# Optimization experiments

Measured on AMD Instinct MI355X. Metric: run time of the kernel, lower is better.

The kernel has to match this reference:

```python
import jax, jax.numpy as jnp
import numpy as np

# Model hyperparams (must match init_kwargs)
N_CATEGORIES = 1000
EMBED_DIM = 128
N_DEMAND = 8
HIDDEN = 128
B, L, N_ITEMS = 16, 50, 8192


def setup_inputs() -> dict:
    key = jax.random.key(0)
    ks = jax.random.split(key, 12)
    inp = {}
    inp["input"] = jax.random.randint(ks[0], (B, L), 0, N_CATEGORIES)
    inp["candidate_pool_category"] = jax.random.randint(ks[1], (N_ITEMS,), 0, N_CATEGORIES)
    inp["session_last_catgy_index"] = jax.random.randint(ks[2], (B,), 0, L)
    inp["mask_catgy"] = jnp.ones((B, L), dtype=jnp.float32)
    # Learned parameters (torch Linear stored as (in, out) so y = x @ W + b)
    emb = 0.02 * jax.random.normal(ks[3], (N_CATEGORIES, EMBED_DIM), dtype=jnp.float32)
    inp["emb_table"] = emb.at[0].set(0.0)  # padding_idx=0
    sd = 1.0 / np.sqrt(EMBED_DIM)
    sh = 1.0 / np.sqrt(HIDDEN)
    inp["Wd"] = sd * jax.random.normal(ks[4], (EMBED_DIM, N_DEMAND * HIDDEN), dtype=jnp.float32)
    inp["Wk"] = sd * jax.random.normal(ks[5], (EMBED_DIM, HIDDEN), dtype=jnp.float32)
    inp["bk"] = sd * jax.random.normal(ks[6], (HIDDEN,), dtype=jnp.float32)
    inp["W1"] = (1.0 / np.sqrt(2 * HIDDEN)) * jax.random.normal(ks[7], (2 * HIDDEN, HIDDEN), dtype=jnp.float32)
    inp["b1"] = sh * jax.random.normal(ks[8], (HIDDEN,), dtype=jnp.float32)
    inp["w_score"] = sh * jax.random.normal(ks[9], (HIDDEN,), dtype=jnp.float32)
    inp["Wc"] = sh * jax.random.normal(ks[10], (HIDDEN, N_CATEGORIES), dtype=jnp.float32)
    inp["bc"] = sh * jax.random.normal(ks[11], (N_CATEGORIES,), dtype=jnp.float32)
    return inp


def reference(input, candidate_pool_category, session_last_catgy_index, mask_catgy,
              emb_table, Wd, Wk, bk, W1, b1, w_score, Wc, bc):
    B_, L_ = input.shape
    h = Wk.shape[1]
    D = Wd.shape[1] // h

    emb = emb_table[input]                      # (B, L, d)  (dropout = identity at eval)
    emb_cand = emb_table[candidate_pool_category]  # (N, d)

    hidden_key = emb @ Wk + bk                  # (B, L, h)
    hidden_demand = (emb @ Wd).reshape(B_, L_, D, h)
    # demand_agg == 'exp': log(sum(exp(.), axis=seq))
    agg = jax.nn.logsumexp(hidden_demand, axis=1)   # (B, D, h)

    # demand similarity loss: mean off-diagonal cosine similarity between demands
    hn = agg / (jnp.linalg.norm(agg, axis=-1, keepdims=True) + 1e-12)
    sim = jnp.einsum('bdh,beh->bde', hn, hn)
    off = sim * (1.0 - jnp.eye(D, dtype=sim.dtype))
    demand_sim_loss = jnp.sum(off) / (B_ * D * (D - 1))

    hidden_key_cand = emb_cand @ Wk + bk        # (N, h)

    # MLP score: cat([demand, key]) @ W1 == demand @ W1[:h] + key @ W1[h:]
    Wd1, Wk1 = W1[:h], W1[h:]
    pd = agg @ Wd1                              # (B, D, h)
    pk = hidden_key @ Wk1                       # (B, L, h)
    s = jax.nn.relu(pd[:, None, :, :] + pk[:, :, None, :] + b1)  # (B, L, D, h)
    # torch does .view(B, D, L) on a contiguous (B, L, D) tensor -> raw reshape (kept faithful)
    demand_score = (s @ w_score).reshape(B_, D, L_)              # (B, D, L)

    pkc = hidden_key_cand @ Wk1                 # (N, h)
    sc = jax.nn.relu(pd[:, :, None, :] + pkc[None, None, :, :] + b1)  # (B, D, N, h)
    demand_score_candidate = sc @ w_score       # (B, D, N)

    # predict_catgy ('mlp'): linear head over aggregated demand (reconstructed; body truncated in source)
    catgy_score = agg @ Wc + bc                 # (B, D, n_categories)

    return (catgy_score, demand_score, demand_score_candidate, emb, emb_cand, demand_sim_loss)
```

## Files before the change

kernel.cpp:

```cpp
#include <hip/hip_runtime.h>
#include <hip/hip_bf16.h>

#define NB 16
#define NL 50
#define ND 8
#define NH 128
#define NC 1000
#define NI 8192

#define OFF_CAT  0
#define OFF_DS   128000
#define OFF_DSC  134400
#define OFF_EMB  1182976
#define OFF_EMBC 1285376
#define OFF_LOSS 2333952

#define WS_SPART 0
#define WS_PK    81920
#define WS_PKCT  184320
#define WS_WP    1232896
#define WS_BP    1249280
#define WS_AGG   1249408
#define WS_PD2   1265792

__global__ __launch_bounds__(256) void k_stage0(
    const int* __restrict__ inp, const float* __restrict__ emb_table,
    const float* __restrict__ Wd, const float* __restrict__ Wk,
    const float* __restrict__ bk, const float* __restrict__ W1,
    float* __restrict__ ws_wp, float* __restrict__ ws_bp,
    float* __restrict__ ws_spart, float* __restrict__ out_loss)
{
    const int bx = blockIdx.x;
    const int t = threadIdx.x;
    const int c = t & 127, g = t >> 7;
    __shared__ __align__(16) float smem[1536];

    if (bx < 64) {
        float* wk_s = smem;
        const float* __restrict__ Wk1 = W1 + 128 * 128;
        const int r0 = bx * 2;
        wk_s[t] = Wk[(r0 + g) * 128 + c];
        __syncthreads();
        float a = 0.f;
        for (int k = 0; k < 128; k += 4) {
            #pragma unroll
            for (int j = 0; j < 4; ++j)
                a = fmaf(wk_s[g * 128 + k + j], Wk1[(k + j) * 128 + c], a);
        }
        ws_wp[(r0 + g) * 128 + c] = a;
    } else if (bx == 64) {
        float* wk_s = smem;
        const float* __restrict__ Wk1 = W1 + 128 * 128;
        if (t < 128) wk_s[t] = bk[t];
        __syncthreads();
        if (t < 128) {
            float a = 0.f;
            for (int k = 0; k < 128; k += 4) {
                #pragma unroll
                for (int j = 0; j < 4; ++j)
                    a = fmaf(wk_s[k + j], Wk1[(k + j) * 128 + t], a);
            }
            ws_bp[t] = a;
        }
        if (t == 0) out_loss[0] = 0.f;
    } else {
        const int idx = bx - 65;
        const int bd = idx / 5, chunk = idx % 5;
        const int b = bd >> 3, d = bd & 7;
        float* se = smem;
        float* ss = smem + 1280;
        for (int ii = t; ii < 1280; ii += 256) {
            const int row = ii >> 7, col = ii & 127;
            const int cat = inp[b * NL + chunk * 10 + row];
            se[ii] = emb_table[cat * 128 + col];
        }
        __syncthreads();
        const float* __restrict__ wp = Wd + d * 128 + c;
        float acc[5] = {0.f, 0.f, 0.f, 0.f, 0.f};
        const int l0 = g * 5;
        for (int k = 0; k < 128; k += 4) {
            const float w0 = wp[(k + 0) * 1024], w1 = wp[(k + 1) * 1024];
            const float w2 = wp[(k + 2) * 1024], w3 = wp[(k + 3) * 1024];
            #pragma unroll
            for (int li = 0; li < 5; ++li) {
                const float4 e4 = *reinterpret_cast<const float4*>(&se[(l0 + li) * 128 + k]);
                acc[li] = fmaf(e4.w, w3, fmaf(e4.z, w2, fmaf(e4.y, w1, fmaf(e4.x, w0, acc[li]))));
            }
        }
        float s = 0.f;
        #pragma unroll
        for (int li = 0; li < 5; ++li) s += expf(acc[li]);
        ss[g * 128 + c] = s;
        __syncthreads();
        if (g == 0)
            ws_spart[(bd * 5 + chunk) * 128 + c] = ss[c] + ss[128 + c];
    }
}

__global__ __launch_bounds__(256) void k_stage1(
    const int* __restrict__ inp, const int* __restrict__ cand,
    const float* __restrict__ emb_table, const float* __restrict__ W1,
    const float* __restrict__ b1, const float* __restrict__ Wc,
    const float* __restrict__ bc, const float* __restrict__ ws_wp,
    const float* __restrict__ ws_bp, const float* __restrict__ ws_spart,
    float* __restrict__ out_emb, float* __restrict__ out_embc,
    float* __restrict__ out_cat, float* __restrict__ ws_pk,
    float* __restrict__ ws_pkcT, float* __restrict__ ws_agg,
    float* __restrict__ ws_pd2)
{
    const int bx = blockIdx.x;
    const int t = threadIdx.x;
    const int c = t & 127, g = t >> 7;
    __shared__ __align__(16) float smem[2176];

    if (bx < 100) {
        const int r0 = bx * 8;
        float* e_s = smem;
        #pragma unroll
        for (int r = 0; r < 4; ++r) {
            const int gr = g * 4 + r;
            const int cat = inp[r0 + gr];
            const float v = emb_table[cat * 128 + c];
            e_s[gr * 128 + c] = v;
            out_emb[(r0 + gr) * 128 + c] = v;
        }
        __syncthreads();
        const float bpv = ws_bp[c];
        float acc[4] = {bpv, bpv, bpv, bpv};
        for (int k = 0; k < 128; k += 4) {
            const float w0 = ws_wp[(k + 0) * 128 + c], w1 = ws_wp[(k + 1) * 128 + c];
            const float w2 = ws_wp[(k + 2) * 128 + c], w3 = ws_wp[(k + 3) * 128 + c];
            #pragma unroll
            for (int r = 0; r < 4; ++r) {
                const float4 e4 = *reinterpret_cast<const float4*>(&e_s[(g * 4 + r) * 128 + k]);
                acc[r] = fmaf(e4.w, w3, fmaf(e4.z, w2, fmaf(e4.y, w1, fmaf(e4.x, w0, acc[r]))));
            }
        }
        #pragma unroll
        for (int r = 0; r < 4; ++r) ws_pk[(r0 + g * 4 + r) * 128 + c] = acc[r];
    } else if (bx < 612) {
        const int i0 = (bx - 100) * 16;
        float* e_s = smem;
        #pragma unroll
        for (int r = 0; r < 8; ++r) {
            const int gr = g * 8 + r;
            const int cat = cand[i0 + gr];
            const float v = emb_table[cat * 128 + c];
            e_s[gr * 128 + c] = v;
            out_embc[(i0 + gr) * 128 + c] = v;
        }
        __syncthreads();
        const float bpv = ws_bp[c];
        float acc[8];
        #pragma unroll
        for (int r = 0; r < 8; ++r) acc[r] = bpv;
        for (int k = 0; k < 128; k += 4) {
            const float w0 = ws_wp[(k + 0) * 128 + c], w1 = ws_wp[(k + 1) * 128 + c];
            const float w2 = ws_wp[(k + 2) * 128 + c], w3 = ws_wp[(k + 3) * 128 + c];
            #pragma unroll
            for (int r = 0; r < 8; ++r) {
                const float4 e4 = *reinterpret_cast<const float4*>(&e_s[(g * 8 + r) * 128 + k]);
                acc[r] = fmaf(e4.w, w3, fmaf(e4.z, w2, fmaf(e4.y, w1, fmaf(e4.x, w0, acc[r]))));
            }
        }
        __syncthreads();
        float* tb = smem;
        #pragma unroll
        for (int r = 0; r < 8; ++r) tb[(g * 8 + r) * 132 + c] = acc[r];
        __syncthreads();
        #pragma unroll
        for (int p = 0; p < 2; ++p) {
            const int h = p * 64 + (t >> 2);
            const int ib = (t & 3) * 4;
            const float4 v = make_float4(tb[(ib + 0) * 132 + h], tb[(ib + 1) * 132 + h],
                                         tb[(ib + 2) * 132 + h], tb[(ib + 3) * 132 + h]);
            *reinterpret_cast<float4*>(&ws_pkcT[(size_t)h * NI + i0 + ib]) = v;
        }
    } else {
        const int bd = bx - 612;
        float* a_s = smem;
        if (g == 0) {
            float s = 0.f;
            #pragma unroll
            for (int ch = 0; ch < 5; ++ch) s += ws_spart[(bd * 5 + ch) * 128 + c];
            const float av = logf(s);
            a_s[c] = av;
            ws_agg[bd * 128 + c] = av;
        }
        __syncthreads();
        if (g == 0) {
            float acc = b1[c];
            for (int k = 0; k < 128; k += 4) {
                acc = fmaf(a_s[k + 0], W1[(k + 0) * 128 + c], acc);
                acc = fmaf(a_s[k + 1], W1[(k + 1) * 128 + c], acc);
                acc = fmaf(a_s[k + 2], W1[(k + 2) * 128 + c], acc);
                acc = fmaf(a_s[k + 3], W1[(k + 3) * 128 + c], acc);
            }
            ws_pd2[bd * 128 + c] = acc;
        }
        float acc4[4];
        int   col4[4];
        #pragma unroll
        for (int j = 0; j < 4; ++j) {
            const int col = t + j * 256;
            col4[j] = (col < NC) ? col : (NC - 1);
            acc4[j] = bc[col4[j]];
        }
        for (int k = 0; k < 128; ++k) {
            const float av = a_s[k];
            const float* wr = Wc + (size_t)k * NC;
            #pragma unroll
            for (int j = 0; j < 4; ++j) acc4[j] = fmaf(av, wr[col4[j]], acc4[j]);
        }
        #pragma unroll
        for (int j = 0; j < 4; ++j) {
            const int col = t + j * 256;
            if (col < NC) out_cat[bd * NC + col] = acc4[j];
        }
    }
}

__global__ __launch_bounds__(256) void k_tail3(
    const float* __restrict__ ws_agg, const float* __restrict__ ws_pd2,
    const float* __restrict__ ws_pk, const float* __restrict__ ws_pkcT,
    const float* __restrict__ w_score, float* __restrict__ out_ds,
    float* __restrict__ out_dsc, float* __restrict__ out_loss)
{
    const int bx = blockIdx.x;
    const int t = threadIdx.x;
    __shared__ __align__(16) float smem[928];
    float* pd_s = smem;
    float* ws_s = smem + 512;
    float* sp   = smem + 640;
    float* aux  = smem + 896;

    if (bx < 1024) {
        const int ichunk = bx & 31, rh = (bx >> 5) & 1, b = bx >> 6;
        const int r0 = b * 8 + rh * 4;
        const int i = ichunk * 256 + t;
        for (int j = t; j < 512; j += 256) pd_s[j] = ws_pd2[r0 * 128 + j];
        if (t < 128) ws_s[t] = w_score[t];
        __syncthreads();
        float a0 = 0.f, a1 = 0.f, a2 = 0.f, a3 = 0.f;
        const float* __restrict__ pc0 = ws_pkcT + i;
        float4 pv = make_float4(pc0[0], pc0[NI], pc0[2 * NI], pc0[3 * NI]);
        for (int h = 0; h < 128; h += 4) {
            const float4 cur = pv;
            if (h + 4 < 128) {
                const float* __restrict__ pn = ws_pkcT + (size_t)(h + 4) * NI + i;
                pv = make_float4(pn[0], pn[NI], pn[2 * NI], pn[3 * NI]);
            }
            const float4 w4 = *reinterpret_cast<const float4*>(&ws_s[h]);
            const float4 p0 = *reinterpret_cast<const float4*>(&pd_s[h]);
            const float4 p1 = *reinterpret_cast<const float4*>(&pd_s[128 + h]);
            const float4 p2 = *reinterpret_cast<const float4*>(&pd_s[256 + h]);
            const float4 p3 = *reinterpret_cast<const float4*>(&pd_s[384 + h]);
            a0 = fmaf(fmaxf(p0.x + cur.x, 0.f), w4.x, a0);
            a0 = fmaf(fmaxf(p0.y + cur.y, 0.f), w4.y, a0);
            a0 = fmaf(fmaxf(p0.z + cur.z, 0.f), w4.z, a0);
            a0 = fmaf(fmaxf(p0.w + cur.w, 0.f), w4.w, a0);
            a1 = fmaf(fmaxf(p1.x + cur.x, 0.f), w4.x, a1);
            a1 = fmaf(fmaxf(p1.y + cur.y, 0.f), w4.y, a1);
            a1 = fmaf(fmaxf(p1.z + cur.z, 0.f), w4.z, a1);
            a1 = fmaf(fmaxf(p1.w + cur.w, 0.f), w4.w, a1);
            a2 = fmaf(fmaxf(p2.x + cur.x, 0.f), w4.x, a2);
            a2 = fmaf(fmaxf(p2.y + cur.y, 0.f), w4.y, a2);
            a2 = fmaf(fmaxf(p2.z + cur.z, 0.f), w4.z, a2);
            a2 = fmaf(fmaxf(p2.w + cur.w, 0.f), w4.w, a2);
            a3 = fmaf(fmaxf(p3.x + cur.x, 0.f), w4.x, a3);
            a3 = fmaf(fmaxf(p3.y + cur.y, 0.f), w4.y, a3);
            a3 = fmaf(fmaxf(p3.z + cur.z, 0.f), w4.z, a3);
            a3 = fmaf(fmaxf(p3.w + cur.w, 0.f), w4.w, a3);
        }
        out_dsc[(size_t)(r0 + 0) * NI + i] = a0;
        out_dsc[(size_t)(r0 + 1) * NI + i] = a1;
        out_dsc[(size_t)(r0 + 2) * NI + i] = a2;
        out_dsc[(size_t)(r0 + 3) * NI + i] = a3;
    } else if (bx < 1824) {
        const int bl = bx - 1024;
        const int b = bl / 50, l = bl % 50;
        const int c = t & 127, g = t >> 7;
        const int w = t >> 6, lane = t & 63;
        float* red = aux;
        const float pkv = ws_pk[(size_t)bl * 128 + c];
        const float wv = w_score[c];
        #pragma unroll
        for (int r = 0; r < 4; ++r) {
            const int d = g * 4 + r;
            float v = fmaxf(ws_pd2[(b * 8 + d) * 128 + c] + pkv, 0.f) * wv;
            v += __shfl_down(v, 32); v += __shfl_down(v, 16); v += __shfl_down(v, 8);
            v += __shfl_down(v, 4);  v += __shfl_down(v, 2);  v += __shfl_down(v, 1);
            if (lane == 0) red[w * 4 + r] = v;
        }
        __syncthreads();
        if (t < 8) {
            const int gg = t >> 2, rr = t & 3;
            out_ds[b * 400 + l * 8 + t] = red[(2 * gg) * 4 + rr] + red[(2 * gg + 1) * 4 + rr];
        }
    } else {
        const int b = bx - 1824;
        const int c = t & 127, g = t >> 7;
        const int w = t >> 6, lane = t & 63;
        float* normp = aux;
        float* wred  = aux + 16;
        float a[4];
        #pragma unroll
        for (int r = 0; r < 4; ++r) a[r] = ws_agg[(b * 8 + g * 4 + r) * 128 + c];
        #pragma unroll
        for (int r = 0; r < 4; ++r) {
            float s = a[r] * a[r];
            s += __shfl_down(s, 32); s += __shfl_down(s, 16); s += __shfl_down(s, 8);
            s += __shfl_down(s, 4);  s += __shfl_down(s, 2);  s += __shfl_down(s, 1);
            if (lane == 0) normp[w * 4 + r] = s;
        }
        __syncthreads();
        float Sp = 0.f;
        #pragma unroll
        for (int r = 0; r < 4; ++r) {
            const float nsq = normp[(2 * g) * 4 + r] + normp[(2 * g + 1) * 4 + r];
            const float iv = 1.f / (sqrtf(nsq) + 1e-12f);
            Sp = fmaf(a[r], iv, Sp);
        }
        sp[g * 128 + c] = Sp;
        __syncthreads();
        float p = 0.f;
        if (t < 128) {
            const float S = sp[c] + sp[128 + c];
            p = S * S;
        }
        p += __shfl_down(p, 32); p += __shfl_down(p, 16); p += __shfl_down(p, 8);
        p += __shfl_down(p, 4);  p += __shfl_down(p, 2);  p += __shfl_down(p, 1);
        if (lane == 0) wred[w] = p;
        __syncthreads();
        if (t == 0) {
            float corr = 0.f;
            #pragma unroll
            for (int d = 0; d < 8; ++d) {
                const float nsq = normp[(2 * (d >> 2)) * 4 + (d & 3)] +
                                  normp[(2 * (d >> 2) + 1) * 4 + (d & 3)];
                const float iv = 1.f / (sqrtf(nsq) + 1e-12f);
                corr = fmaf(nsq, iv * iv, corr);
            }
            atomicAdd(out_loss,
                      (wred[0] + wred[1] + wred[2] + wred[3] - corr) * (1.0f / 896.0f));
        }
    }
}

extern "C" void kernel_launch(void* const* d_in, const int* in_sizes, int n_in,
                              void* d_out, int out_size, void* d_ws, size_t ws_size,
                              hipStream_t stream)
{
    const int*   input     = (const int*)d_in[0];
    const int*   cand      = (const int*)d_in[1];
    const float* emb_table = (const float*)d_in[4];
    const float* Wd        = (const float*)d_in[5];
    const float* Wk        = (const float*)d_in[6];
    const float* bk        = (const float*)d_in[7];
    const float* W1        = (const float*)d_in[8];
    const float* b1        = (const float*)d_in[9];
    const float* w_score   = (const float*)d_in[10];
    const float* Wc        = (const float*)d_in[11];
    const float* bc        = (const float*)d_in[12];

    float* out = (float*)d_out;
    float* out_cat  = out + OFF_CAT;
    float* out_ds   = out + OFF_DS;
    float* out_dsc  = out + OFF_DSC;
    float* out_emb  = out + OFF_EMB;
    float* out_embc = out + OFF_EMBC;
    float* out_loss = out + OFF_LOSS;

    float* ws       = (float*)d_ws;
    float* ws_spart = ws + WS_SPART;
    float* ws_pk    = ws + WS_PK;
    float* ws_pkcT  = ws + WS_PKCT;
    float* ws_wp    = ws + WS_WP;
    float* ws_bp    = ws + WS_BP;
    float* ws_agg   = ws + WS_AGG;
    float* ws_pd2   = ws + WS_PD2;

    k_stage0<<<705, 256, 0, stream>>>(input, emb_table, Wd, Wk, bk, W1,
                                      ws_wp, ws_bp, ws_spart, out_loss);
    k_stage1<<<740, 256, 0, stream>>>(input, cand, emb_table, W1, b1, Wc, bc,
                                      ws_wp, ws_bp, ws_spart,
                                      out_emb, out_embc, out_cat,
                                      ws_pk, ws_pkcT, ws_agg, ws_pd2);
    k_tail3<<<1840, 256, 0, stream>>>(ws_agg, ws_pd2, ws_pk, ws_pkcT, w_score,
                                      out_ds, out_dsc, out_loss);
}
```

Before: 119.7 us.

## Fuse three kernels into one persistent kernel with software grid barriers

Merges the three stage kernels into a single launch of 1024 blocks. Two atomic-counter grid barriers, reset by a memset before the launch, separate the former stages, and the tail stage loops its 1840 work items over the fixed grid. This removes the launch gaps between kernels. In exchange it adds barrier spin cost, and it deadlocks unless all 1024 blocks are resident at once (launch bounds request 4 blocks per CU).

```diff
diff --git a/kernel.cpp b/kernel.cpp
--- a/kernel.cpp
+++ b/kernel.cpp
@@ -22,18 +22,41 @@
 #define WS_BP    1249280
 #define WS_AGG   1249408
 #define WS_PD2   1265792
-
-__global__ __launch_bounds__(256) void k_stage0(
-    const int* __restrict__ inp, const float* __restrict__ emb_table,
-    const float* __restrict__ Wd, const float* __restrict__ Wk,
-    const float* __restrict__ bk, const float* __restrict__ W1,
-    float* __restrict__ ws_wp, float* __restrict__ ws_bp,
-    float* __restrict__ ws_spart, float* __restrict__ out_loss)
+#define WS_BAR   1282176
+
+#define GRID_N 1024
+
+__device__ __forceinline__ void grid_barrier(int* cnt) {
+    __syncthreads();
+    if (threadIdx.x == 0) {
+        __threadfence();
+        atomicAdd(cnt, 1);
+        while (atomicAdd(cnt, 0) < GRID_N)
+            __builtin_amdgcn_s_sleep(2);
+        __threadfence();
+    }
+    __syncthreads();
+}
+
+__global__ __launch_bounds__(256, 4) void k_all(
+    const int* __restrict__ inp, const int* __restrict__ cand,
+    const float* __restrict__ emb_table, const float* __restrict__ Wd,
+    const float* __restrict__ Wk, const float* __restrict__ bk,
+    const float* __restrict__ W1, const float* __restrict__ b1,
+    const float* __restrict__ w_score, const float* __restrict__ Wc,
+    const float* __restrict__ bc,
+    float* __restrict__ out_emb, float* __restrict__ out_embc,
+    float* __restrict__ out_cat, float* __restrict__ out_ds,
+    float* __restrict__ out_dsc, float* __restrict__ out_loss,
+    float* __restrict__ ws_pk, float* __restrict__ ws_pkcT,
+    float* __restrict__ ws_spart, float* __restrict__ ws_wp,
+    float* __restrict__ ws_bp, float* __restrict__ ws_agg,
+    float* __restrict__ ws_pd2, int* __restrict__ bar)
 {
     const int bx = blockIdx.x;
     const int t = threadIdx.x;
     const int c = t & 127, g = t >> 7;
-    __shared__ __align__(16) float smem[1536];
+    __shared__ __align__(16) float smem[2176];
 
     if (bx < 64) {
         float* wk_s = smem;
@@ -63,7 +86,7 @@
             ws_bp[t] = a;
         }
         if (t == 0) out_loss[0] = 0.f;
-    } else {
+    } else if (bx < 705) {
         const int idx = bx - 65;
         const int bd = idx / 5, chunk = idx % 5;
         const int b = bd >> 3, d = bd & 7;
@@ -95,23 +118,8 @@
         if (g == 0)
             ws_spart[(bd * 5 + chunk) * 128 + c] = ss[c] + ss[128 + c];
     }
-}
-
-__global__ __launch_bounds__(256) void k_stage1(
-    const int* __restrict__ inp, const int* __restrict__ cand,
-    const float* __restrict__ emb_table, const float* __restrict__ W1,
-    const float* __restrict__ b1, const float* __restrict__ Wc,
-    const float* __restrict__ bc, const float* __restrict__ ws_wp,
-    const float* __restrict__ ws_bp, const float* __restrict__ ws_spart,
-    float* __restrict__ out_emb, float* __restrict__ out_embc,
-    float* __restrict__ out_cat, float* __restrict__ ws_pk,
-    float* __restrict__ ws_pkcT, float* __restrict__ ws_agg,
-    float* __restrict__ ws_pd2)
-{
-    const int bx = blockIdx.x;
-    const int t = threadIdx.x;
-    const int c = t & 127, g = t >> 7;
-    __shared__ __align__(16) float smem[2176];
+
+    grid_barrier(&bar[0]);
 
     if (bx < 100) {
         const int r0 = bx * 8;
@@ -176,7 +184,7 @@
                                          tb[(ib + 2) * 132 + h], tb[(ib + 3) * 132 + h]);
             *reinterpret_cast<float4*>(&ws_pkcT[(size_t)h * NI + i0 + ib]) = v;
         }
-    } else {
+    } else if (bx < 740) {
         const int bd = bx - 612;
         float* a_s = smem;
         if (g == 0) {
@@ -218,131 +226,124 @@
             if (col < NC) out_cat[bd * NC + col] = acc4[j];
         }
     }
-}
-
-__global__ __launch_bounds__(256) void k_tail3(
-    const float* __restrict__ ws_agg, const float* __restrict__ ws_pd2,
-    const float* __restrict__ ws_pk, const float* __restrict__ ws_pkcT,
-    const float* __restrict__ w_score, float* __restrict__ out_ds,
-    float* __restrict__ out_dsc, float* __restrict__ out_loss)
-{
-    const int bx = blockIdx.x;
-    const int t = threadIdx.x;
-    __shared__ __align__(16) float smem[928];
+
+    grid_barrier(&bar[16]);
+
     float* pd_s = smem;
     float* ws_s = smem + 512;
     float* sp   = smem + 640;
     float* aux  = smem + 896;
 
-    if (bx < 1024) {
-        const int ichunk = bx & 31, rh = (bx >> 5) & 1, b = bx >> 6;
-        const int r0 = b * 8 + rh * 4;
-        const int i = ichunk * 256 + t;
-        for (int j = t; j < 512; j += 256) pd_s[j] = ws_pd2[r0 * 128 + j];
-        if (t < 128) ws_s[t] = w_score[t];
-        __syncthreads();
-        float a0 = 0.f, a1 = 0.f, a2 = 0.f, a3 = 0.f;
-        const float* __restrict__ pc0 = ws_pkcT + i;
-        float4 pv = make_float4(pc0[0], pc0[NI], pc0[2 * NI], pc0[3 * NI]);
-        for (int h = 0; h < 128; h += 4) {
-            const float4 cur = pv;
-            if (h + 4 < 128) {
-                const float* __restrict__ pn = ws_pkcT + (size_t)(h + 4) * NI + i;
-                pv = make_float4(pn[0], pn[NI], pn[2 * NI], pn[3 * NI]);
-            }
-            const float4 w4 = *reinterpret_cast<const float4*>(&ws_s[h]);
-            const float4 p0 = *reinterpret_cast<const float4*>(&pd_s[h]);
-            const float4 p1 = *reinterpret_cast<const float4*>(&pd_s[128 + h]);
-            const float4 p2 = *reinterpret_cast<const float4*>(&pd_s[256 + h]);
-            const float4 p3 = *reinterpret_cast<const float4*>(&pd_s[384 + h]);
-            a0 = fmaf(fmaxf(p0.x + cur.x, 0.f), w4.x, a0);
-            a0 = fmaf(fmaxf(p0.y + cur.y, 0.f), w4.y, a0);
-            a0 = fmaf(fmaxf(p0.z + cur.z, 0.f), w4.z, a0);
-            a0 = fmaf(fmaxf(p0.w + cur.w, 0.f), w4.w, a0);
-            a1 = fmaf(fmaxf(p1.x + cur.x, 0.f), w4.x, a1);
-            a1 = fmaf(fmaxf(p1.y + cur.y, 0.f), w4.y, a1);
-            a1 = fmaf(fmaxf(p1.z + cur.z, 0.f), w4.z, a1);
-            a1 = fmaf(fmaxf(p1.w + cur.w, 0.f), w4.w, a1);
-            a2 = fmaf(fmaxf(p2.x + cur.x, 0.f), w4.x, a2);
-            a2 = fmaf(fmaxf(p2.y + cur.y, 0.f), w4.y, a2);
-            a2 = fmaf(fmaxf(p2.z + cur.z, 0.f), w4.z, a2);
-            a2 = fmaf(fmaxf(p2.w + cur.w, 0.f), w4.w, a2);
-            a3 = fmaf(fmaxf(p3.x + cur.x, 0.f), w4.x, a3);
-            a3 = fmaf(fmaxf(p3.y + cur.y, 0.f), w4.y, a3);
-            a3 = fmaf(fmaxf(p3.z + cur.z, 0.f), w4.z, a3);
-            a3 = fmaf(fmaxf(p3.w + cur.w, 0.f), w4.w, a3);
-        }
-        out_dsc[(size_t)(r0 + 0) * NI + i] = a0;
-        out_dsc[(size_t)(r0 + 1) * NI + i] = a1;
-        out_dsc[(size_t)(r0 + 2) * NI + i] = a2;
-        out_dsc[(size_t)(r0 + 3) * NI + i] = a3;
-    } else if (bx < 1824) {
-        const int bl = bx - 1024;
-        const int b = bl / 50, l = bl % 50;
-        const int c = t & 127, g = t >> 7;
-        const int w = t >> 6, lane = t & 63;
-        float* red = aux;
-        const float pkv = ws_pk[(size_t)bl * 128 + c];
-        const float wv = w_score[c];
-        #pragma unroll
-        for (int r = 0; r < 4; ++r) {
-            const int d = g * 4 + r;
-            float v = fmaxf(ws_pd2[(b * 8 + d) * 128 + c] + pkv, 0.f) * wv;
-            v += __shfl_down(v, 32); v += __shfl_down(v, 16); v += __shfl_down(v, 8);
-            v += __shfl_down(v, 4);  v += __shfl_down(v, 2);  v += __shfl_down(v, 1);
-            if (lane == 0) red[w * 4 + r] = v;
-        }
-        __syncthreads();
-        if (t < 8) {
-            const int gg = t >> 2, rr = t & 3;
-            out_ds[b * 400 + l * 8 + t] = red[(2 * gg) * 4 + rr] + red[(2 * gg + 1) * 4 + rr];
-        }
-    } else {
-        const int b = bx - 1824;
-        const int c = t & 127, g = t >> 7;
-        const int w = t >> 6, lane = t & 63;
-        float* normp = aux;
-        float* wred  = aux + 16;
-        float a[4];
-        #pragma unroll
-        for (int r = 0; r < 4; ++r) a[r] = ws_agg[(b * 8 + g * 4 + r) * 128 + c];
-        #pragma unroll
-        for (int r = 0; r < 4; ++r) {
-            float s = a[r] * a[r];
-            s += __shfl_down(s, 32); s += __shfl_down(s, 16); s += __shfl_down(s, 8);
-            s += __shfl_down(s, 4);  s += __shfl_down(s, 2);  s += __shfl_down(s, 1);
-            if (lane == 0) normp[w * 4 + r] = s;
-        }
-        __syncthreads();
-        float Sp = 0.f;
-        #pragma unroll
-        for (int r = 0; r < 4; ++r) {
-            const float nsq = normp[(2 * g) * 4 + r] + normp[(2 * g + 1) * 4 + r];
-            const float iv = 1.f / (sqrtf(nsq) + 1e-12f);
-            Sp = fmaf(a[r], iv, Sp);
-        }
-        sp[g * 128 + c] = Sp;
-        __syncthreads();
-        float p = 0.f;
-        if (t < 128) {
-            const float S = sp[c] + sp[128 + c];
-            p = S * S;
-        }
-        p += __shfl_down(p, 32); p += __shfl_down(p, 16); p += __shfl_down(p, 8);
-        p += __shfl_down(p, 4);  p += __shfl_down(p, 2);  p += __shfl_down(p, 1);
-        if (lane == 0) wred[w] = p;
-        __syncthreads();
-        if (t == 0) {
-            float corr = 0.f;
-            #pragma unroll
-            for (int d = 0; d < 8; ++d) {
-                const float nsq = normp[(2 * (d >> 2)) * 4 + (d & 3)] +
-                                  normp[(2 * (d >> 2) + 1) * 4 + (d & 3)];
+    for (int r2 = bx; r2 < 1840; r2 += GRID_N) {
+        __syncthreads();
+        if (r2 < 1024) {
+            const int ichunk = r2 & 31, rh = (r2 >> 5) & 1, b = r2 >> 6;
+            const int r0 = b * 8 + rh * 4;
+            const int i = ichunk * 256 + t;
+            for (int j = t; j < 512; j += 256) pd_s[j] = ws_pd2[r0 * 128 + j];
+            if (t < 128) ws_s[t] = w_score[t];
+            __syncthreads();
+            float a0 = 0.f, a1 = 0.f, a2 = 0.f, a3 = 0.f;
+            const float* __restrict__ pc0 = ws_pkcT + i;
+            float4 pv = make_float4(pc0[0], pc0[NI], pc0[2 * NI], pc0[3 * NI]);
+            for (int h = 0; h < 128; h += 4) {
+                const float4 cur = pv;
+                if (h + 4 < 128) {
+                    const float* __restrict__ pn = ws_pkcT + (size_t)(h + 4) * NI + i;
+                    pv = make_float4(pn[0], pn[NI], pn[2 * NI], pn[3 * NI]);
+                }
+                const float4 w4 = *reinterpret_cast<const float4*>(&ws_s[h]);
+                const float4 p0 = *reinterpret_cast<const float4*>(&pd_s[h]);
+                const float4 p1 = *reinterpret_cast<const float4*>(&pd_s[128 + h]);
+                const float4 p2 = *reinterpret_cast<const float4*>(&pd_s[256 + h]);
+                const float4 p3 = *reinterpret_cast<const float4*>(&pd_s[384 + h]);
+                a0 = fmaf(fmaxf(p0.x + cur.x, 0.f), w4.x, a0);
+                a0 = fmaf(fmaxf(p0.y + cur.y, 0.f), w4.y, a0);
+                a0 = fmaf(fmaxf(p0.z + cur.z, 0.f), w4.z, a0);
+                a0 = fmaf(fmaxf(p0.w + cur.w, 0.f), w4.w, a0);
+                a1 = fmaf(fmaxf(p1.x + cur.x, 0.f), w4.x, a1);
+                a1 = fmaf(fmaxf(p1.y + cur.y, 0.f), w4.y, a1);
+                a1 = fmaf(fmaxf(p1.z + cur.z, 0.f), w4.z, a1);
+                a1 = fmaf(fmaxf(p1.w + cur.w, 0.f), w4.w, a1);
+                a2 = fmaf(fmaxf(p2.x + cur.x, 0.f), w4.x, a2);
+                a2 = fmaf(fmaxf(p2.y + cur.y, 0.f), w4.y, a2);
+                a2 = fmaf(fmaxf(p2.z + cur.z, 0.f), w4.z, a2);
+                a2 = fmaf(fmaxf(p2.w + cur.w, 0.f), w4.w, a2);
+                a3 = fmaf(fmaxf(p3.x + cur.x, 0.f), w4.x, a3);
+                a3 = fmaf(fmaxf(p3.y + cur.y, 0.f), w4.y, a3);
+                a3 = fmaf(fmaxf(p3.z + cur.z, 0.f), w4.z, a3);
+                a3 = fmaf(fmaxf(p3.w + cur.w, 0.f), w4.w, a3);
+            }
+            out_dsc[(size_t)(r0 + 0) * NI + i] = a0;
+            out_dsc[(size_t)(r0 + 1) * NI + i] = a1;
+            out_dsc[(size_t)(r0 + 2) * NI + i] = a2;
+            out_dsc[(size_t)(r0 + 3) * NI + i] = a3;
+        } else if (r2 < 1824) {
+            const int bl = r2 - 1024;
+            const int b = bl / 50, l = bl % 50;
+            const int w = t >> 6, lane = t & 63;
+            float* red = aux;
+            const float pkv = ws_pk[(size_t)bl * 128 + c];
+            const float wv = w_score[c];
+            #pragma unroll
+            for (int r = 0; r < 4; ++r) {
+                const int d = g * 4 + r;
+                float v = fmaxf(ws_pd2[(b * 8 + d) * 128 + c] + pkv, 0.f) * wv;
+                v += __shfl_down(v, 32); v += __shfl_down(v, 16); v += __shfl_down(v, 8);
+                v += __shfl_down(v, 4);  v += __shfl_down(v, 2);  v += __shfl_down(v, 1);
+                if (lane == 0) red[w * 4 + r] = v;
+            }
+            __syncthreads();
+            if (t < 8) {
+                const int gg = t >> 2, rr = t & 3;
+                out_ds[b * 400 + l * 8 + t] = red[(2 * gg) * 4 + rr] + red[(2 * gg + 1) * 4 + rr];
+            }
+        } else {
+            const int b = r2 - 1824;
+            const int w = t >> 6, lane = t & 63;
+            float* normp = aux;
+            float* wred  = aux + 16;
+            float a[4];
+            #pragma unroll
+            for (int r = 0; r < 4; ++r) a[r] = ws_agg[(b * 8 + g * 4 + r) * 128 + c];
+            #pragma unroll
+            for (int r = 0; r < 4; ++r) {
+                float s = a[r] * a[r];
+                s += __shfl_down(s, 32); s += __shfl_down(s, 16); s += __shfl_down(s, 8);
+                s += __shfl_down(s, 4);  s += __shfl_down(s, 2);  s += __shfl_down(s, 1);
+                if (lane == 0) normp[w * 4 + r] = s;
+            }
+            __syncthreads();
+            float Sp = 0.f;
+            #pragma unroll
+            for (int r = 0; r < 4; ++r) {
+                const float nsq = normp[(2 * g) * 4 + r] + normp[(2 * g + 1) * 4 + r];
                 const float iv = 1.f / (sqrtf(nsq) + 1e-12f);
-                corr = fmaf(nsq, iv * iv, corr);
-            }
-            atomicAdd(out_loss,
-                      (wred[0] + wred[1] + wred[2] + wred[3] - corr) * (1.0f / 896.0f));
+                Sp = fmaf(a[r], iv, Sp);
+            }
+            sp[g * 128 + c] = Sp;
+            __syncthreads();
+            float p = 0.f;
+            if (t < 128) {
+                const float S = sp[c] + sp[128 + c];
+                p = S * S;
+            }
+            p += __shfl_down(p, 32); p += __shfl_down(p, 16); p += __shfl_down(p, 8);
+            p += __shfl_down(p, 4);  p += __shfl_down(p, 2);  p += __shfl_down(p, 1);
+            if (lane == 0) wred[w] = p;
+            __syncthreads();
+            if (t == 0) {
+                float corr = 0.f;
+                #pragma unroll
+                for (int d = 0; d < 8; ++d) {
+                    const float nsq = normp[(2 * (d >> 2)) * 4 + (d & 3)] +
+                                      normp[(2 * (d >> 2) + 1) * 4 + (d & 3)];
+                    const float iv = 1.f / (sqrtf(nsq) + 1e-12f);
+                    corr = fmaf(nsq, iv * iv, corr);
+                }
+                atomicAdd(out_loss,
+                          (wred[0] + wred[1] + wred[2] + wred[3] - corr) * (1.0f / 896.0f));
+            }
         }
     }
 }
@@ -379,13 +380,13 @@
     float* ws_bp    = ws + WS_BP;
     float* ws_agg   = ws + WS_AGG;
     float* ws_pd2   = ws + WS_PD2;
-
-    k_stage0<<<705, 256, 0, stream>>>(input, emb_table, Wd, Wk, bk, W1,
-                                      ws_wp, ws_bp, ws_spart, out_loss);
-    k_stage1<<<740, 256, 0, stream>>>(input, cand, emb_table, W1, b1, Wc, bc,
-                                      ws_wp, ws_bp, ws_spart,
-                                      out_emb, out_embc, out_cat,
-                                      ws_pk, ws_pkcT, ws_agg, ws_pd2);
-    k_tail3<<<1840, 256, 0, stream>>>(ws_agg, ws_pd2, ws_pk, ws_pkcT, w_score,
-                                      out_ds, out_dsc, out_loss);
+    int*   bar      = (int*)(ws + WS_BAR);
+
+    hipMemsetAsync(bar, 0, 128, stream);
+    k_all<<<GRID_N, 256, 0, stream>>>(input, cand, emb_table, Wd, Wk, bk, W1, b1,
+                                      w_score, Wc, bc,
+                                      out_emb, out_embc, out_cat, out_ds,
+                                      out_dsc, out_loss,
+                                      ws_pk, ws_pkcT, ws_spart, ws_wp, ws_bp,
+                                      ws_agg, ws_pd2, bar);
 }
```

Measured after the change: 374.2 us. 3.13x slower.
